# Kernel tuning notes

Measured on AMD Instinct MI355X. Metric: run time of the kernel, lower is better.

The kernel has to match this reference:

```python
import jax, jax.numpy as jnp
import numpy as np

R = 16
ALPHA = 32.0
SCALING = ALPHA / R


def setup_inputs() -> dict:
    key = jax.random.key(0)
    ks = jax.random.split(key, 6)
    B, T, C, O, E = 16, 1500, 1024, 1024, 8
    x = jax.random.normal(ks[0], (B, T, C), dtype=jnp.float32)
    # gate weights per batch element (e.g. softmax-like, but module accepts any)
    w = jax.random.uniform(ks[1], (B, E), dtype=jnp.float32)
    W_base = jax.random.normal(ks[2], (O, C), dtype=jnp.float32) * 0.02
    b_base = jax.random.normal(ks[3], (O,), dtype=jnp.float32) * 0.02
    As = jax.random.normal(ks[4], (E, R, C), dtype=jnp.float32) * 0.02
    Bs = jax.random.normal(ks[5], (E, O, R), dtype=jnp.float32) * 0.02
    return {"x": x, "w": w, "W_base": W_base, "b_base": b_base, "As": As, "Bs": Bs}


def reference(x, w, W_base, b_base, As, Bs):
    # base linear: (B,T,C) @ (C,O) + b
    out = jnp.einsum('btc,oc->bto', x, W_base) + b_base
    # per-expert low-rank: h[b,t,e,r] = x[b,t,:] @ A_e^T
    h = jnp.einsum('btc,erc->bter', x, As)          # (B,T,E,R)
    # y[b,t,e,o] = h @ B_e^T ; gate-weighted sum over experts
    lora = jnp.einsum('bter,eor,be->bto', h, Bs, w)  # (B,T,O)
    return out + lora * SCALING
```

## Files before the change

kernel.cpp:

```cpp
#include <hip/hip_runtime.h>
#include <stdint.h>
#include <stddef.h>


#define B_ 16
#define T_ 1500
#define C_ 1024
#define O_ 1024
#define E_ 8
#define R_ 16
#define ER 128
#define KK 1152
#define BT 24000
#define SCALING 2.0f

typedef __bf16 bf16x8 __attribute__((ext_vector_type(8)));
typedef float f32x4 __attribute__((ext_vector_type(4)));
typedef unsigned short u16;
typedef u16 u16x8 __attribute__((ext_vector_type(8)));

__device__ inline u16 f2bf(float f) {
  union { float f; unsigned u; } v; v.f = f;
  unsigned u = v.u;
  u += 0x7fff + ((u >> 16) & 1);
  return (u16)(u >> 16);
}

#define GLL(gp, lp)                                                            \
  __builtin_amdgcn_global_load_lds(                                            \
      (const __attribute__((address_space(1))) void*)(gp),                     \
      (__attribute__((address_space(3))) void*)(lp), 16, 0, 0)

__global__ __launch_bounds__(256) void prep_w(const float* __restrict__ Wb,
                                              const float* __restrict__ Bs,
                                              const float* __restrict__ As,
                                              u16* __restrict__ wp,
                                              u16* __restrict__ ap) {
  int idx = blockIdx.x * 256 + threadIdx.x;
  if (idx < O_ * KK) {
    int o = idx / KK;
    int k = idx - o * KK;
    float v;
    if (k < C_) {
      v = Wb[o * C_ + k];
    } else {
      int j = k - C_;
      v = Bs[((j >> 4) * O_ + o) * R_ + (j & 15)];
    }
    wp[idx] = f2bf(v);
  } else {
    int a = idx - O_ * KK;
    ap[a] = f2bf(As[a]);
  }
}

__global__ __launch_bounds__(256) void cvt(const float* __restrict__ x,
                                           u16* __restrict__ xp) {
  const int t0 = blockIdx.x * 256 + threadIdx.x;
#pragma unroll
  for (int u = 0; u < 6; ++u) {
    const int chunk = u * 512000 + t0;
    const int row = chunk >> 7;
    const int cc = (chunk & 127) * 8;
    const float4 v0 = *(const float4*)&x[(size_t)row * C_ + cc];
    const float4 v1 = *(const float4*)&x[(size_t)row * C_ + cc + 4];
    u16x8 o;
    o[0] = f2bf(v0.x); o[1] = f2bf(v0.y); o[2] = f2bf(v0.z); o[3] = f2bf(v0.w);
    o[4] = f2bf(v1.x); o[5] = f2bf(v1.y); o[6] = f2bf(v1.z); o[7] = f2bf(v1.w);
    *(u16x8*)&xp[(size_t)row * KK + cc] = o;
  }
}

__global__ __launch_bounds__(256) void h_gemm(const u16* __restrict__ xp,
                                              const u16* __restrict__ ab,
                                              const float* __restrict__ w,
                                              u16* __restrict__ xpo) {
  const int mt = blockIdx.x;
  const int tid = threadIdx.x, lane = tid & 63, wv = tid >> 6;
  const int wrow = wv & 1, wcol = wv >> 1, l15 = lane & 15, quad = lane >> 4;
  const int s7 = l15 & 7;

  __shared__ u16 lA[64 * 64];
  __shared__ u16 lB[128 * 64];

  const u16* gA = xp + (size_t)mt * 64 * KK;

  f32x4 acc[2][4];
#pragma unroll
  for (int i = 0; i < 2; ++i)
#pragma unroll
    for (int j = 0; j < 4; ++j) acc[i][j] = (f32x4){0.f, 0.f, 0.f, 0.f};

  int arow[2], ako[2], brow[4], bko[4];
#pragma unroll
  for (int c = 0; c < 2; ++c) {
    int idx = c * 256 + tid;
    arow[c] = idx >> 3;
    ako[c] = (((idx & 7) ^ (arow[c] & 7)) << 3);
  }
#pragma unroll
  for (int c = 0; c < 4; ++c) {
    int idx = c * 256 + tid;
    brow[c] = idx >> 3;
    bko[c] = (((idx & 7) ^ (brow[c] & 7)) << 3);
  }

  for (int kt = 0; kt < C_ / 64; ++kt) {
    const int k0 = kt * 64;
#pragma unroll
    for (int c = 0; c < 2; ++c)
      GLL(gA + (size_t)arow[c] * KK + k0 + ako[c], &lA[(c * 256 + tid) * 8]);
#pragma unroll
    for (int c = 0; c < 4; ++c)
      GLL(ab + brow[c] * C_ + k0 + bko[c], &lB[(c * 256 + tid) * 8]);
    __syncthreads();
#pragma unroll
    for (int kk = 0; kk < 2; ++kk) {
      const int ko = (((kk * 4 + quad) ^ s7) << 3);
      bf16x8 af[2], bfr[4];
#pragma unroll
      for (int i = 0; i < 2; ++i)
        af[i] = *(const bf16x8*)&lA[(wrow * 32 + i * 16 + l15) * 64 + ko];
#pragma unroll
      for (int j = 0; j < 4; ++j)
        bfr[j] = *(const bf16x8*)&lB[(wcol * 64 + j * 16 + l15) * 64 + ko];
#pragma unroll
      for (int i = 0; i < 2; ++i)
#pragma unroll
        for (int j = 0; j < 4; ++j)
          acc[i][j] = __builtin_amdgcn_mfma_f32_16x16x32_bf16(af[i], bfr[j], acc[i][j], 0, 0, 0);
    }
    __syncthreads();
  }

#pragma unroll
  for (int j = 0; j < 4; ++j) {
    const int col = wcol * 64 + j * 16 + l15;
    const int e = wcol * 4 + j;
#pragma unroll
    for (int i = 0; i < 2; ++i) {
#pragma unroll
      for (int rr = 0; rr < 4; ++rr) {
        const int row = mt * 64 + wrow * 32 + i * 16 + quad * 4 + rr;
        const int b = row / T_;
        xpo[(size_t)row * KK + C_ + col] = f2bf(acc[i][j][rr] * (SCALING * w[b * E_ + e]));
      }
    }
  }
}

__global__ __launch_bounds__(256) void main_gemm(const u16* __restrict__ xp,
                                                 const u16* __restrict__ wp,
                                                 const float* __restrict__ bb,
                                                 float* __restrict__ out) {
  const int id = blockIdx.x;
  const int mt = ((id >> 6) << 3) | (id & 7);
  const int nt = (id >> 3) & 7;
  if (mt >= 188) return;
  const int tid = threadIdx.x, lane = tid & 63, wv = tid >> 6;
  const int wrow = wv & 1, wcol = wv >> 1, l15 = lane & 15, quad = lane >> 4;
  const int kx = quad ^ (l15 & 3) ^ ((l15 >> 2) & 3);

  __shared__ u16 lA[128 * 32];
  __shared__ u16 lB[128 * 32];
  const u16* gA = xp + (size_t)mt * 128 * KK;
  const u16* gB = wp + (size_t)nt * 128 * KK;

  f32x4 acc[4][4];
#pragma unroll
  for (int i = 0; i < 4; ++i)
#pragma unroll
    for (int j = 0; j < 4; ++j) acc[i][j] = (f32x4){0.f, 0.f, 0.f, 0.f};

  const int idx0 = tid, idx1 = 256 + tid;
  const int r0 = idx0 >> 2, kc0 = (idx0 & 3) ^ (r0 & 3) ^ ((r0 >> 2) & 3);
  const int r1 = idx1 >> 2, kc1 = (idx1 & 3) ^ (r1 & 3) ^ ((r1 >> 2) & 3);

  for (int kt = 0; kt < KK / 32; ++kt) {
    const int k0 = kt * 32;
    GLL(gA + (size_t)r0 * KK + k0 + kc0 * 8, &lA[idx0 * 8]);
    GLL(gA + (size_t)r1 * KK + k0 + kc1 * 8, &lA[idx1 * 8]);
    GLL(gB + (size_t)r0 * KK + k0 + kc0 * 8, &lB[idx0 * 8]);
    GLL(gB + (size_t)r1 * KK + k0 + kc1 * 8, &lB[idx1 * 8]);
    __syncthreads();
    bf16x8 af[4], bfr[4];
#pragma unroll
    for (int i = 0; i < 4; ++i) {
      af[i] = *(const bf16x8*)&lA[(wrow * 64 + i * 16 + l15) * 32 + kx * 8];
      bfr[i] = *(const bf16x8*)&lB[(wcol * 64 + i * 16 + l15) * 32 + kx * 8];
    }
#pragma unroll
    for (int i = 0; i < 4; ++i)
#pragma unroll
      for (int j = 0; j < 4; ++j)
        acc[i][j] = __builtin_amdgcn_mfma_f32_16x16x32_bf16(af[i], bfr[j], acc[i][j], 0, 0, 0);
    __syncthreads();
  }

#pragma unroll
  for (int j = 0; j < 4; ++j) {
    const int col = nt * 128 + wcol * 64 + j * 16 + l15;
    const float bias = bb[col];
#pragma unroll
    for (int i = 0; i < 4; ++i) {
#pragma unroll
      for (int rr = 0; rr < 4; ++rr) {
        const int row = mt * 128 + wrow * 64 + i * 16 + quad * 4 + rr;
        if (row < BT) out[(size_t)row * O_ + col] = acc[i][j][rr] + bias;
      }
    }
  }
}

extern "C" void kernel_launch(void* const* d_in, const int* in_sizes, int n_in,
                              void* d_out, int out_size, void* d_ws, size_t ws_size,
                              hipStream_t stream) {
  const float* x = (const float*)d_in[0];
  const float* w = (const float*)d_in[1];
  const float* Wb = (const float*)d_in[2];
  const float* bb = (const float*)d_in[3];
  const float* As = (const float*)d_in[4];
  const float* Bs = (const float*)d_in[5];
  float* out = (float*)d_out;

  u16* xp = (u16*)d_ws;
  u16* wp = xp + (size_t)BT * KK;
  u16* ap = wp + (size_t)O_ * KK;

  prep_w<<<(O_ * KK + ER * C_) / 256, 256, 0, stream>>>(Wb, Bs, As, wp, ap);
  cvt<<<2000, 256, 0, stream>>>(x, xp);
  h_gemm<<<375, 256, 0, stream>>>(xp, ap, w, xp);
  main_gemm<<<1536, 256, 0, stream>>>(xp, wp, bb, out);
}
```

Baseline: 292.4 us.

## Double-buffer main GEMM with K=64 tiles and async prefetch pipeline

Rewrites the main GEMM loop to use K-tiles of 64 with two LDS buffers, prefetching the tile two steps ahead via global_load_lds and explicit vmcnt waits. This overlaps global-to-LDS traffic with MFMA work and halves the number of barrier rounds. It also remaps block IDs to an XCD-aware tile order, launches exactly 1504 blocks, and adds s_setprio around the MFMA block. LDS use doubles to 64KB per block, which caps occupancy at two blocks per CU.

```diff
diff --git a/kernel.cpp b/kernel.cpp
--- a/kernel.cpp
+++ b/kernel.cpp
@@ -12,6 +12,7 @@
 #define ER 128
 #define KK 1152
 #define BT 24000
+#define NKT 18
 #define SCALING 2.0f
 
 typedef __bf16 bf16x8 __attribute__((ext_vector_type(8)));
@@ -149,20 +150,21 @@
   }
 }
 
-__global__ __launch_bounds__(256) void main_gemm(const u16* __restrict__ xp,
-                                                 const u16* __restrict__ wp,
-                                                 const float* __restrict__ bb,
-                                                 float* __restrict__ out) {
+__global__ __launch_bounds__(256, 2) void main_gemm(const u16* __restrict__ xp,
+                                                    const u16* __restrict__ wp,
+                                                    const float* __restrict__ bb,
+                                                    float* __restrict__ out) {
   const int id = blockIdx.x;
-  const int mt = ((id >> 6) << 3) | (id & 7);
-  const int nt = (id >> 3) & 7;
-  if (mt >= 188) return;
+  const int g = (id & 7) * 188 + (id >> 3);
+  const int mt = g >> 3;
+  const int nt = g & 7;
   const int tid = threadIdx.x, lane = tid & 63, wv = tid >> 6;
-  const int wrow = wv & 1, wcol = wv >> 1, l15 = lane & 15, quad = lane >> 4;
-  const int kx = quad ^ (l15 & 3) ^ ((l15 >> 2) & 3);
-
-  __shared__ u16 lA[128 * 32];
-  __shared__ u16 lB[128 * 32];
+  const int wm = wv >> 1, wn = wv & 1, l15 = lane & 15, quad = lane >> 4;
+  const int s7 = l15 & 7;
+
+  __shared__ u16 lA[2][128 * 64];
+  __shared__ u16 lB[2][128 * 64];
+
   const u16* gA = xp + (size_t)mt * 128 * KK;
   const u16* gB = wp + (size_t)nt * 128 * KK;
 
@@ -172,40 +174,84 @@
 #pragma unroll
     for (int j = 0; j < 4; ++j) acc[i][j] = (f32x4){0.f, 0.f, 0.f, 0.f};
 
-  const int idx0 = tid, idx1 = 256 + tid;
-  const int r0 = idx0 >> 2, kc0 = (idx0 & 3) ^ (r0 & 3) ^ ((r0 >> 2) & 3);
-  const int r1 = idx1 >> 2, kc1 = (idx1 & 3) ^ (r1 & 3) ^ ((r1 >> 2) & 3);
-
-  for (int kt = 0; kt < KK / 32; ++kt) {
-    const int k0 = kt * 32;
-    GLL(gA + (size_t)r0 * KK + k0 + kc0 * 8, &lA[idx0 * 8]);
-    GLL(gA + (size_t)r1 * KK + k0 + kc1 * 8, &lA[idx1 * 8]);
-    GLL(gB + (size_t)r0 * KK + k0 + kc0 * 8, &lB[idx0 * 8]);
-    GLL(gB + (size_t)r1 * KK + k0 + kc1 * 8, &lB[idx1 * 8]);
-    __syncthreads();
-    bf16x8 af[4], bfr[4];
+  const u16* pA[4];
+  const u16* pB[4];
+  int dst[4];
+#pragma unroll
+  for (int c = 0; c < 4; ++c) {
+    int idx = c * 256 + tid;
+    int row = idx >> 3;
+    int ko = (((idx & 7) ^ (row & 7)) << 3);
+    pA[c] = gA + (size_t)row * KK + ko;
+    pB[c] = gB + (size_t)row * KK + ko;
+    dst[c] = idx * 8;
+  }
+
+#pragma unroll
+  for (int c = 0; c < 4; ++c) GLL(pA[c], &lA[0][dst[c]]);
+#pragma unroll
+  for (int c = 0; c < 4; ++c) GLL(pB[c], &lB[0][dst[c]]);
+#pragma unroll
+  for (int c = 0; c < 4; ++c) GLL(pA[c] + 64, &lA[1][dst[c]]);
+#pragma unroll
+  for (int c = 0; c < 4; ++c) GLL(pB[c] + 64, &lB[1][dst[c]]);
+
+#pragma unroll 2
+  for (int t = 0; t < NKT; ++t) {
+    const int cur = t & 1;
+    if (t < NKT - 1) {
+      asm volatile("s_waitcnt vmcnt(8)" ::: "memory");
+    } else {
+      asm volatile("s_waitcnt vmcnt(0)" ::: "memory");
+    }
+    __builtin_amdgcn_sched_barrier(0);
+    __builtin_amdgcn_s_barrier();
+    __builtin_amdgcn_sched_barrier(0);
+
+    bf16x8 af[4][2], bfr[4][2];
+#pragma unroll
+    for (int ks = 0; ks < 2; ++ks) {
+      const int ko = (((ks * 4 + quad) ^ s7) << 3);
+#pragma unroll
+      for (int i = 0; i < 4; ++i) {
+        af[i][ks] = *(const bf16x8*)&lA[cur][(wm * 64 + i * 16 + l15) * 64 + ko];
+        bfr[i][ks] = *(const bf16x8*)&lB[cur][(wn * 64 + i * 16 + l15) * 64 + ko];
+      }
+    }
+    asm volatile("s_waitcnt lgkmcnt(0)" ::: "memory");
+    __builtin_amdgcn_sched_barrier(0);
+    __builtin_amdgcn_s_barrier();
+    __builtin_amdgcn_sched_barrier(0);
+
+    if (t + 2 < NKT) {
+      const int k2 = (t + 2) * 64;
+#pragma unroll
+      for (int c = 0; c < 4; ++c) GLL(pA[c] + k2, &lA[cur][dst[c]]);
+#pragma unroll
+      for (int c = 0; c < 4; ++c) GLL(pB[c] + k2, &lB[cur][dst[c]]);
+    }
+
+    __builtin_amdgcn_s_setprio(1);
+#pragma unroll
+    for (int ks = 0; ks < 2; ++ks)
+#pragma unroll
+      for (int i = 0; i < 4; ++i)
+#pragma unroll
+        for (int j = 0; j < 4; ++j)
+          acc[i][j] = __builtin_amdgcn_mfma_f32_16x16x32_bf16(af[i][ks], bfr[j][ks],
+                                                              acc[i][j], 0, 0, 0);
+    __builtin_amdgcn_s_setprio(0);
+  }
+
+#pragma unroll
+  for (int j = 0; j < 4; ++j) {
+    const int col = nt * 128 + wn * 64 + j * 16 + l15;
+    const float bias = bb[col];
 #pragma unroll
     for (int i = 0; i < 4; ++i) {
-      af[i] = *(const bf16x8*)&lA[(wrow * 64 + i * 16 + l15) * 32 + kx * 8];
-      bfr[i] = *(const bf16x8*)&lB[(wcol * 64 + i * 16 + l15) * 32 + kx * 8];
-    }
-#pragma unroll
-    for (int i = 0; i < 4; ++i)
-#pragma unroll
-      for (int j = 0; j < 4; ++j)
-        acc[i][j] = __builtin_amdgcn_mfma_f32_16x16x32_bf16(af[i], bfr[j], acc[i][j], 0, 0, 0);
-    __syncthreads();
-  }
-
-#pragma unroll
-  for (int j = 0; j < 4; ++j) {
-    const int col = nt * 128 + wcol * 64 + j * 16 + l15;
-    const float bias = bb[col];
-#pragma unroll
-    for (int i = 0; i < 4; ++i) {
 #pragma unroll
       for (int rr = 0; rr < 4; ++rr) {
-        const int row = mt * 128 + wrow * 64 + i * 16 + quad * 4 + rr;
+        const int row = mt * 128 + wm * 64 + i * 16 + quad * 4 + rr;
         if (row < BT) out[(size_t)row * O_ + col] = acc[i][j][rr] + bias;
       }
     }
@@ -230,5 +276,5 @@
   prep_w<<<(O_ * KK + ER * C_) / 256, 256, 0, stream>>>(Wb, Bs, As, wp, ap);
   cvt<<<2000, 256, 0, stream>>>(x, xp);
   h_gemm<<<375, 256, 0, stream>>>(xp, ap, w, xp);
-  main_gemm<<<1536, 256, 0, stream>>>(xp, wp, bb, out);
-}
+  main_gemm<<<1504, 256, 0, stream>>>(xp, wp, bb, out);
+}
```

Result: no change. 290.4 us (-0.7%).

## Rewrite main GEMM with 192x256 tiles, double-buffered LDS and XCD-aware mapping

Applied to the files above, without the earlier changes.

The main GEMM moves from 128x128 tiles with 256 threads and single-buffered 32-wide K steps to 192x256 tiles with 512 threads, 64-wide K steps and double-buffered LDS. Global-to-LDS loads for tile k+2 are issued while MFMAs run on the current tile, and LDS fragment reads are split so half the MFMAs overlap the next reads. Scheduling uses sched barriers and setprio. The block index is remapped so each XCD handles a contiguous range of tiles, which should improve L2 reuse. In exchange, register and LDS use per block grow sharply (about 112 KB LDS), and the row bounds check is dropped because 24000 divides evenly by 192.

```diff
diff --git a/kernel.cpp b/kernel.cpp
--- a/kernel.cpp
+++ b/kernel.cpp
@@ -12,6 +12,7 @@
 #define ER 128
 #define KK 1152
 #define BT 24000
+#define NKT 18
 #define SCALING 2.0f
 
 typedef __bf16 bf16x8 __attribute__((ext_vector_type(8)));
@@ -30,6 +31,8 @@
   __builtin_amdgcn_global_load_lds(                                            \
       (const __attribute__((address_space(1))) void*)(gp),                     \
       (__attribute__((address_space(3))) void*)(lp), 16, 0, 0)
+
+#define SBAR __builtin_amdgcn_sched_barrier(0)
 
 __global__ __launch_bounds__(256) void prep_w(const float* __restrict__ Wb,
                                               const float* __restrict__ Bs,
@@ -149,64 +152,156 @@
   }
 }
 
-__global__ __launch_bounds__(256) void main_gemm(const u16* __restrict__ xp,
-                                                 const u16* __restrict__ wp,
-                                                 const float* __restrict__ bb,
-                                                 float* __restrict__ out) {
+__global__ __launch_bounds__(512, 2) void main_gemm(const u16* __restrict__ xp,
+                                                    const u16* __restrict__ wp,
+                                                    const float* __restrict__ bb,
+                                                    float* __restrict__ out) {
   const int id = blockIdx.x;
-  const int mt = ((id >> 6) << 3) | (id & 7);
-  const int nt = (id >> 3) & 7;
-  if (mt >= 188) return;
+  const int xcd = id & 7, win = id >> 3;
+  const int g = (xcd < 4 ? xcd * 63 : 252 + (xcd - 4) * 62) + win;
+  const int mt = g >> 2;
+  const int nt = g & 3;
   const int tid = threadIdx.x, lane = tid & 63, wv = tid >> 6;
-  const int wrow = wv & 1, wcol = wv >> 1, l15 = lane & 15, quad = lane >> 4;
-  const int kx = quad ^ (l15 & 3) ^ ((l15 >> 2) & 3);
-
-  __shared__ u16 lA[128 * 32];
-  __shared__ u16 lB[128 * 32];
-  const u16* gA = xp + (size_t)mt * 128 * KK;
-  const u16* gB = wp + (size_t)nt * 128 * KK;
-
-  f32x4 acc[4][4];
-#pragma unroll
-  for (int i = 0; i < 4; ++i)
+  const int wm = wv >> 2, wn = wv & 3, l15 = lane & 15, quad = lane >> 4;
+  const int s7 = l15 & 7;
+  const int ko0 = (quad ^ s7) << 3;
+  const int ko1 = ((4 + quad) ^ s7) << 3;
+
+  __shared__ u16 lA[2][192 * 64];
+  __shared__ u16 lB[2][256 * 64];
+
+  const u16* gA = xp + (size_t)mt * 192 * KK;
+  const u16* gB = wp + (size_t)nt * 256 * KK;
+
+  f32x4 acc[6][4];
+#pragma unroll
+  for (int i = 0; i < 6; ++i)
 #pragma unroll
     for (int j = 0; j < 4; ++j) acc[i][j] = (f32x4){0.f, 0.f, 0.f, 0.f};
 
-  const int idx0 = tid, idx1 = 256 + tid;
-  const int r0 = idx0 >> 2, kc0 = (idx0 & 3) ^ (r0 & 3) ^ ((r0 >> 2) & 3);
-  const int r1 = idx1 >> 2, kc1 = (idx1 & 3) ^ (r1 & 3) ^ ((r1 >> 2) & 3);
-
-  for (int kt = 0; kt < KK / 32; ++kt) {
-    const int k0 = kt * 32;
-    GLL(gA + (size_t)r0 * KK + k0 + kc0 * 8, &lA[idx0 * 8]);
-    GLL(gA + (size_t)r1 * KK + k0 + kc1 * 8, &lA[idx1 * 8]);
-    GLL(gB + (size_t)r0 * KK + k0 + kc0 * 8, &lB[idx0 * 8]);
-    GLL(gB + (size_t)r1 * KK + k0 + kc1 * 8, &lB[idx1 * 8]);
-    __syncthreads();
-    bf16x8 af[4], bfr[4];
-#pragma unroll
-    for (int i = 0; i < 4; ++i) {
-      af[i] = *(const bf16x8*)&lA[(wrow * 64 + i * 16 + l15) * 32 + kx * 8];
-      bfr[i] = *(const bf16x8*)&lB[(wcol * 64 + i * 16 + l15) * 32 + kx * 8];
-    }
-#pragma unroll
-    for (int i = 0; i < 4; ++i)
-#pragma unroll
-      for (int j = 0; j < 4; ++j)
-        acc[i][j] = __builtin_amdgcn_mfma_f32_16x16x32_bf16(af[i], bfr[j], acc[i][j], 0, 0, 0);
-    __syncthreads();
-  }
-
+  const u16* pA[3];
+  const u16* pB[4];
+  int dA[3], dB[4];
+#pragma unroll
+  for (int c = 0; c < 3; ++c) {
+    int idx = c * 512 + tid;
+    int row = idx >> 3;
+    pA[c] = gA + (size_t)row * KK + (((idx & 7) ^ (row & 7)) << 3);
+    dA[c] = idx * 8;
+  }
+#pragma unroll
+  for (int c = 0; c < 4; ++c) {
+    int idx = c * 512 + tid;
+    int row = idx >> 3;
+    pB[c] = gB + (size_t)row * KK + (((idx & 7) ^ (row & 7)) << 3);
+    dB[c] = idx * 8;
+  }
+
+#define ROWA(i) ((wm * 96 + (i) * 16 + l15) * 64)
+#define ROWB(j) ((wn * 64 + (j) * 16 + l15) * 64)
+
+#pragma unroll
+  for (int c = 0; c < 3; ++c) GLL(pA[c], &lA[0][dA[c]]);
+#pragma unroll
+  for (int c = 0; c < 4; ++c) GLL(pB[c], &lB[0][dB[c]]);
+#pragma unroll
+  for (int c = 0; c < 3; ++c) GLL(pA[c] + 64, &lA[1][dA[c]]);
+#pragma unroll
+  for (int c = 0; c < 4; ++c) GLL(pB[c] + 64, &lB[1][dB[c]]);
+  asm volatile("s_waitcnt vmcnt(7)" ::: "memory");
+  SBAR;
+  __builtin_amdgcn_s_barrier();
+  SBAR;
+
+  bf16x8 af0[3][2], af1[3][2], bfA[4][2], bfB[4][2];
+#pragma unroll
+  for (int i = 0; i < 3; ++i) {
+    af0[i][0] = *(const bf16x8*)&lA[0][ROWA(i) + ko0];
+    af0[i][1] = *(const bf16x8*)&lA[0][ROWA(i) + ko1];
+  }
 #pragma unroll
   for (int j = 0; j < 4; ++j) {
-    const int col = nt * 128 + wcol * 64 + j * 16 + l15;
+    bfA[j][0] = *(const bf16x8*)&lB[0][ROWB(j) + ko0];
+    bfA[j][1] = *(const bf16x8*)&lB[0][ROWB(j) + ko1];
+  }
+
+#define TILE_BODY(T, CUR, BC, BN_)                                             \
+  {                                                                            \
+    const int t_ = (T);                                                        \
+    _Pragma("unroll")                                                          \
+    for (int i = 0; i < 3; ++i) {                                              \
+      af1[i][0] = *(const bf16x8*)&lA[CUR][ROWA(i + 3) + ko0];                 \
+      af1[i][1] = *(const bf16x8*)&lA[CUR][ROWA(i + 3) + ko1];                 \
+    }                                                                          \
+    __builtin_amdgcn_s_setprio(1);                                             \
+    _Pragma("unroll")                                                          \
+    for (int ks = 0; ks < 2; ++ks)                                             \
+      _Pragma("unroll")                                                        \
+      for (int i = 0; i < 3; ++i)                                              \
+        _Pragma("unroll")                                                      \
+        for (int j = 0; j < 4; ++j)                                            \
+          acc[i][j] = __builtin_amdgcn_mfma_f32_16x16x32_bf16(                 \
+              af0[i][ks], BC[j][ks], acc[i][j], 0, 0, 0);                      \
+    __builtin_amdgcn_s_setprio(0);                                             \
+    asm volatile("s_waitcnt lgkmcnt(0)" ::: "memory");                         \
+    SBAR;                                                                      \
+    __builtin_amdgcn_s_barrier();               \
+    SBAR;                                                                      \
+    if (t_ + 2 < NKT) {                                                        \
+      const int k2 = (t_ + 2) * 64;                                            \
+      _Pragma("unroll")                                                        \
+      for (int c = 0; c < 3; ++c) GLL(pA[c] + k2, &lA[CUR][dA[c]]);            \
+      _Pragma("unroll")                                                        \
+      for (int c = 0; c < 4; ++c) GLL(pB[c] + k2, &lB[CUR][dB[c]]);            \
+      asm volatile("s_waitcnt vmcnt(7)" ::: "memory");                         \
+    } else {                                                                   \
+      asm volatile("s_waitcnt vmcnt(0)" ::: "memory");                         \
+    }                                                                          \
+    SBAR;                                                                      \
+    __builtin_amdgcn_s_barrier();     \
+    SBAR;                                                                      \
+    if (t_ + 1 < NKT) {                                                        \
+      _Pragma("unroll")                                                        \
+      for (int i = 0; i < 3; ++i) {                                            \
+        af0[i][0] = *(const bf16x8*)&lA[CUR ^ 1][ROWA(i) + ko0];               \
+        af0[i][1] = *(const bf16x8*)&lA[CUR ^ 1][ROWA(i) + ko1];               \
+      }                                                                        \
+      _Pragma("unroll")                                                        \
+      for (int j = 0; j < 4; ++j) {                                            \
+        BN_[j][0] = *(const bf16x8*)&lB[CUR ^ 1][ROWB(j) + ko0];               \
+        BN_[j][1] = *(const bf16x8*)&lB[CUR ^ 1][ROWB(j) + ko1];               \
+      }                                                                        \
+    }                                                                          \
+    __builtin_amdgcn_s_setprio(1);                                             \
+    _Pragma("unroll")                                                          \
+    for (int ks = 0; ks < 2; ++ks)                                             \
+      _Pragma("unroll")                                                        \
+      for (int i = 0; i < 3; ++i)                                              \
+        _Pragma("unroll")                                                      \
+        for (int j = 0; j < 4; ++j)                                            \
+          acc[i + 3][j] = __builtin_amdgcn_mfma_f32_16x16x32_bf16(             \
+              af1[i][ks], BC[j][ks], acc[i + 3][j], 0, 0, 0);                  \
+    __builtin_amdgcn_s_setprio(0);                                             \
+  }
+
+  for (int tt = 0; tt < 9; ++tt) {
+    TILE_BODY(2 * tt, 0, bfA, bfB)
+    TILE_BODY(2 * tt + 1, 1, bfB, bfA)
+  }
+#undef TILE_BODY
+#undef ROWA
+#undef ROWB
+
+#pragma unroll
+  for (int j = 0; j < 4; ++j) {
+    const int col = nt * 256 + wn * 64 + j * 16 + l15;
     const float bias = bb[col];
 #pragma unroll
-    for (int i = 0; i < 4; ++i) {
+    for (int i = 0; i < 6; ++i) {
 #pragma unroll
       for (int rr = 0; rr < 4; ++rr) {
-        const int row = mt * 128 + wrow * 64 + i * 16 + quad * 4 + rr;
-        if (row < BT) out[(size_t)row * O_ + col] = acc[i][j][rr] + bias;
+        const int row = mt * 192 + wm * 96 + i * 16 + quad * 4 + rr;
+        out[(size_t)row * O_ + col] = acc[i][j][rr] + bias;
       }
     }
   }
@@ -230,5 +325,5 @@
   prep_w<<<(O_ * KK + ER * C_) / 256, 256, 0, stream>>>(Wb, Bs, As, wp, ap);
   cvt<<<2000, 256, 0, stream>>>(x, xp);
   h_gemm<<<375, 256, 0, stream>>>(xp, ap, w, xp);
-  main_gemm<<<1536, 256, 0, stream>>>(xp, wp, bb, out);
-}
+  main_gemm<<<500, 512, 0, stream>>>(xp, wp, bb, out);
+}
```

Result: faster. 275.4 us (-5.8%).
